# Optimization experiments

Measured on AMD Instinct MI355X. Metric: run time of the kernel, lower is better.

## Reference

```python
import jax, jax.numpy as jnp
import numpy as np

V, H, E = 32000, 8, 32
T, B = 1024, 8

def setup_inputs() -> dict:
    key = jax.random.key(0)
    ks = jax.random.split(key, 11)
    return {
        "x": jax.random.randint(ks[0], (T, B), 0, V),
        "embeddings": jax.random.normal(ks[1], (V, E), jnp.float32),
        "W_x1": jax.random.normal(ks[2], (E, H), jnp.float32),
        "b_x1": jax.random.normal(ks[3], (H,), jnp.float32),
        "W_h1": jax.random.normal(ks[4], (H, H), jnp.float32),
        "b_h1": jax.random.normal(ks[5], (H,), jnp.float32),
        "W_x2": jax.random.normal(ks[6], (E, H), jnp.float32),
        "b_x2": jax.random.normal(ks[7], (H,), jnp.float32),
        "W_h2": jax.random.normal(ks[8], (H, H), jnp.float32),
        "b_h2": jax.random.normal(ks[9], (H,), jnp.float32),
        "output": jax.random.normal(ks[10], (2 * H, V), jnp.float32),
    }

def _run_rnn(xs, Wx, bx, Wh, bh):
    # xs: [T, B, E]. Emit the hidden state BEFORE consuming x_t (matches torch loop:
    # total_h[t] = h, then h = sigmoid(...)). The last update is computed but unused,
    # exactly like the original loop's `break` only skips an unneeded step.
    Bsz = xs.shape[1]
    Hh = Wh.shape[0]
    def step(h, xe):
        h_new = jax.nn.sigmoid(xe @ Wx + bx + h @ Wh + bh)
        return h_new, h
    h0 = jnp.zeros((Bsz, Hh), xs.dtype)
    _, hs = jax.lax.scan(step, h0, xs)
    return hs  # [T, B, H]

def reference(x, embeddings, W_x1, b_x1, W_h1, b_h1, W_x2, b_x2, W_h2, b_h2, output):
    enc = embeddings[x]  # [T, B, E]
    h1 = _run_rnn(enc, W_x1, b_x1, W_h1, b_h1)                       # forward direction
    h2 = jnp.flip(_run_rnn(jnp.flip(enc, 0), W_x2, b_x2, W_h2, b_h2), 0)  # backward direction
    total_h = jnp.concatenate([h1, h2], axis=2)  # [T, B, 2H]
    logits = total_h @ output                    # [T, B, V]
    return jax.nn.log_softmax(logits, axis=2)
```

## Files before the change

### kernel.cpp

```cpp
#include <hip/hip_runtime.h>
#include <math.h>

#if __has_builtin(__builtin_amdgcn_exp2f)
#define EXP2F(x) __builtin_amdgcn_exp2f(x)
#else
#define EXP2F(x) exp2f(x)
#endif

#if __has_builtin(__builtin_amdgcn_logf)
#define LOG2F(x) __builtin_amdgcn_logf(x)
#else
#define LOG2F(x) log2f(x)
#endif

#if __has_builtin(__builtin_amdgcn_rcpf)
#define RCPF(x) __builtin_amdgcn_rcpf(x)
#else
#define RCPF(x) (1.0f / (x))
#endif

#define L2E 1.44269504088896340736f
#define LN2 0.69314718055994530942f

constexpr int V = 32000;
constexpr int H = 8;
constexpr int E = 32;
constexpr int T = 1024;
constexpr int B = 8;
constexpr int TB = T * B;
constexpr int V4 = V / 4;

__global__ __launch_bounds__(256) void proj_kernel(
    const int* __restrict__ x, const float* __restrict__ emb,
    const float* __restrict__ Wx1, const float* __restrict__ bx1,
    const float* __restrict__ bh1,
    const float* __restrict__ Wx2, const float* __restrict__ bx2,
    const float* __restrict__ bh2,
    float* __restrict__ pre1, float* __restrict__ pre2) {
  int i = blockIdx.x * 256 + threadIdx.x;
  int dir = i >> 16;
  int j = i & 65535;
  int h = j & 7;
  int tb = j >> 3;
  int idx = x[tb];
  const float* e = emb + (size_t)idx * E;
  const float* Wx = dir ? Wx2 : Wx1;
  float sum = dir ? (bx2[h] + bh2[h]) : (bx1[h] + bh1[h]);
#pragma unroll
  for (int e0 = 0; e0 < E; ++e0) sum = fmaf(e[e0], Wx[e0 * H + h], sum);
  (dir ? pre2 : pre1)[j] = sum;
}

__global__ __launch_bounds__(128) void rnn_kernel(
    const float* __restrict__ pre1, const float* __restrict__ pre2,
    const float* __restrict__ Wh1, const float* __restrict__ Wh2,
    float* __restrict__ th ) {
  const int tid = threadIdx.x;
  const int dir = tid >> 6;
  const int lane = tid & 63;
  const int b = lane >> 3;
  const int k = lane & 7;
  const float* pre = dir ? pre2 : pre1;
  const float* Wh = dir ? Wh2 : Wh1;

  float w[8];
#pragma unroll
  for (int j = 0; j < 8; ++j) w[j] = Wh[j * H + k];

  float h = 0.f;
  float cur[8], nxt[8];
#pragma unroll
  for (int u = 0; u < 8; ++u) {
    int s = u;
    int tt = dir ? (T - 1 - s) : s;
    cur[u] = pre[tt * 64 + lane];
  }
  for (int blk = 0; blk < T / 8; ++blk) {
    int base = blk * 8;
    if (blk < T / 8 - 1) {
#pragma unroll
      for (int u = 0; u < 8; ++u) {
        int s = base + 8 + u;
        int tt = dir ? (T - 1 - s) : s;
        nxt[u] = pre[tt * 64 + lane];
      }
    }
#pragma unroll
    for (int u = 0; u < 8; ++u) {
      int s = base + u;
      int tt = dir ? (T - 1 - s) : s;
      th[(tt * B + b) * (2 * H) + dir * H + k] = h;
      float acc = cur[u];
#pragma unroll
      for (int j = 0; j < 8; ++j) {
        float hj = __shfl(h, (lane & 56) | j, 64);
        acc = fmaf(hj, w[j], acc);
      }
      h = RCPF(1.0f + EXP2F(acc * -L2E));
    }
#pragma unroll
    for (int u = 0; u < 8; ++u) cur[u] = nxt[u];
  }
}

__global__ __launch_bounds__(256) void logits_kernel(
    const float* __restrict__ th, const float* __restrict__ Wout,
    float* __restrict__ out) {
  const int tid = threadIdx.x;
  const int row0 = blockIdx.x * 16;

  __shared__ float4 th4[16][4];
  __shared__ float red_m[16][4], red_l[16][4];
  __shared__ float sS[16];

  if (tid < 64) {
    th4[tid >> 2][tid & 3] = ((const float4*)th)[row0 * 4 + tid];
  }
  __syncthreads();

  const float4* W4 = (const float4*)Wout;

  float m[16], l[16];
#pragma unroll
  for (int r = 0; r < 16; ++r) { m[r] = -INFINITY; l[r] = 0.f; }

  for (int v4 = tid; v4 < V4; v4 += 256) {
    float4 w[16];
#pragma unroll
    for (int kk = 0; kk < 16; ++kk) w[kk] = W4[(size_t)kk * V4 + v4];
#pragma unroll
    for (int r = 0; r < 16; ++r) {
      float4 c0 = th4[r][0], c1 = th4[r][1], c2 = th4[r][2], c3 = th4[r][3];
      float cc[16] = {c0.x, c0.y, c0.z, c0.w, c1.x, c1.y, c1.z, c1.w,
                      c2.x, c2.y, c2.z, c2.w, c3.x, c3.y, c3.z, c3.w};
      float ax = 0.f, ay = 0.f, az = 0.f, aw = 0.f;
#pragma unroll
      for (int kk = 0; kk < 16; ++kk) {
        ax = fmaf(w[kk].x, cc[kk], ax);
        ay = fmaf(w[kk].y, cc[kk], ay);
        az = fmaf(w[kk].z, cc[kk], az);
        aw = fmaf(w[kk].w, cc[kk], aw);
      }
      float mx = fmaxf(fmaxf(ax, ay), fmaxf(az, aw));
      float nm = fmaxf(m[r], mx);
      float sc = EXP2F((m[r] - nm) * L2E);
      float s = EXP2F((ax - nm) * L2E) + EXP2F((ay - nm) * L2E) +
                EXP2F((az - nm) * L2E) + EXP2F((aw - nm) * L2E);
      l[r] = fmaf(l[r], sc, s);
      m[r] = nm;
    }
  }

  const int wid = tid >> 6, ln = tid & 63;
#pragma unroll
  for (int r = 0; r < 16; ++r) {
    float mm = m[r], ll = l[r];
#pragma unroll
    for (int off = 32; off > 0; off >>= 1) {
      float om = __shfl_xor(mm, off, 64);
      float ol = __shfl_xor(ll, off, 64);
      float nm = fmaxf(mm, om);
      ll = ll * EXP2F((mm - nm) * L2E) + ol * EXP2F((om - nm) * L2E);
      mm = nm;
    }
    if (ln == 0) { red_m[r][wid] = mm; red_l[r][wid] = ll; }
  }
  __syncthreads();
  if (tid < 16) {
    float mm = red_m[tid][0], ll = red_l[tid][0];
#pragma unroll
    for (int i2 = 1; i2 < 4; ++i2) {
      float om = red_m[tid][i2], ol = red_l[tid][i2];
      float nm = fmaxf(mm, om);
      ll = ll * EXP2F((mm - nm) * L2E) + ol * EXP2F((om - nm) * L2E);
      mm = nm;
    }
    sS[tid] = mm + LOG2F(ll) * LN2;
  }
  __syncthreads();

  float4* out4 = (float4*)out;
  for (int v4 = tid; v4 < V4; v4 += 256) {
    float4 w[16];
#pragma unroll
    for (int kk = 0; kk < 16; ++kk) w[kk] = W4[(size_t)kk * V4 + v4];
#pragma unroll
    for (int r = 0; r < 16; ++r) {
      float4 c0 = th4[r][0], c1 = th4[r][1], c2 = th4[r][2], c3 = th4[r][3];
      float cc[16] = {c0.x, c0.y, c0.z, c0.w, c1.x, c1.y, c1.z, c1.w,
                      c2.x, c2.y, c2.z, c2.w, c3.x, c3.y, c3.z, c3.w};
      float ax = 0.f, ay = 0.f, az = 0.f, aw = 0.f;
#pragma unroll
      for (int kk = 0; kk < 16; ++kk) {
        ax = fmaf(w[kk].x, cc[kk], ax);
        ay = fmaf(w[kk].y, cc[kk], ay);
        az = fmaf(w[kk].z, cc[kk], az);
        aw = fmaf(w[kk].w, cc[kk], aw);
      }
      float S = sS[r];
      float4 o;
      o.x = ax - S; o.y = ay - S; o.z = az - S; o.w = aw - S;
      out4[(size_t)(row0 + r) * V4 + v4] = o;
    }
  }
}

extern "C" void kernel_launch(void* const* d_in, const int* in_sizes, int n_in,
                              void* d_out, int out_size, void* d_ws, size_t ws_size,
                              hipStream_t stream) {
  const int* x = (const int*)d_in[0];
  const float* emb = (const float*)d_in[1];
  const float* Wx1 = (const float*)d_in[2];
  const float* bx1 = (const float*)d_in[3];
  const float* Wh1 = (const float*)d_in[4];
  const float* bh1 = (const float*)d_in[5];
  const float* Wx2 = (const float*)d_in[6];
  const float* bx2 = (const float*)d_in[7];
  const float* Wh2 = (const float*)d_in[8];
  const float* bh2 = (const float*)d_in[9];
  const float* Wout = (const float*)d_in[10];
  float* out = (float*)d_out;

  float* ws = (float*)d_ws;
  float* pre1 = ws;
  float* pre2 = ws + TB * H;
  float* th = ws + 2 * TB * H;

  proj_kernel<<<512, 256, 0, stream>>>(x, emb, Wx1, bx1, bh1, Wx2, bx2, bh2,
                                       pre1, pre2);
  rnn_kernel<<<1, 128, 0, stream>>>(pre1, pre2, Wh1, Wh2, th);
  logits_kernel<<<TB / 16, 256, 0, stream>>>(th, Wout, out);
}
```

Baseline: 2.528 ms.

## Compute RNN step per-thread without shuffles, add nontemporal logits stores and occupancy hint

The serial RNN kernel now has each lane hold the whole 8-element hidden state for one batch row. It computes the 8x8 matvec locally instead of exchanging values with 8 cross-lane shuffles per step, and the prefetch depth drops from 8 to 4 steps. The logits kernel gets a min-blocks-per-CU launch bound of 3 and writes its large output with nontemporal stores to avoid polluting cache. The tradeoffs are 8x redundant work across lanes, more register pressure in the RNN kernel, and a possible register spill caused by the launch bound in the logits kernel.

```diff
diff --git a/kernel.cpp b/kernel.cpp
--- a/kernel.cpp
+++ b/kernel.cpp
@@ -21,6 +21,8 @@
 
 #define L2E 1.44269504088896340736f
 #define LN2 0.69314718055994530942f
+
+typedef float floatx4 __attribute__((ext_vector_type(4)));
 
 constexpr int V = 32000;
 constexpr int H = 8;
@@ -58,52 +60,87 @@
   const int tid = threadIdx.x;
   const int dir = tid >> 6;
   const int lane = tid & 63;
-  const int b = lane >> 3;
-  const int k = lane & 7;
-  const float* pre = dir ? pre2 : pre1;
+  const int b = lane & 7;
+  const int sel = (lane >> 3) & 1;
+  const float4* pre4 = (const float4*)(dir ? pre2 : pre1);
   const float* Wh = dir ? Wh2 : Wh1;
-
-  float w[8];
-#pragma unroll
-  for (int j = 0; j < 8; ++j) w[j] = Wh[j * H + k];
-
-  float h = 0.f;
-  float cur[8], nxt[8];
-#pragma unroll
-  for (int u = 0; u < 8; ++u) {
+  float4* th4 = (float4*)th;
+
+  float w[8][8];
+#pragma unroll
+  for (int i = 0; i < 8; ++i)
+#pragma unroll
+    for (int j = 0; j < 8; ++j) w[i][j] = Wh[i * H + j];
+
+  float h0 = 0.f, h1 = 0.f, h2 = 0.f, h3 = 0.f;
+  float h4 = 0.f, h5 = 0.f, h6 = 0.f, h7 = 0.f;
+
+  constexpr int PF = 4;
+  float4 cur[PF][2], nxt[PF][2];
+
+#pragma unroll
+  for (int u = 0; u < PF; ++u) {
     int s = u;
     int tt = dir ? (T - 1 - s) : s;
-    cur[u] = pre[tt * 64 + lane];
-  }
-  for (int blk = 0; blk < T / 8; ++blk) {
-    int base = blk * 8;
-    if (blk < T / 8 - 1) {
-#pragma unroll
-      for (int u = 0; u < 8; ++u) {
-        int s = base + 8 + u;
+    int a = tt * 16 + b * 2;
+    cur[u][0] = pre4[a];
+    cur[u][1] = pre4[a + 1];
+  }
+
+  for (int blk = 0; blk < T / PF; ++blk) {
+    int base = blk * PF;
+    if (blk < T / PF - 1) {
+#pragma unroll
+      for (int u = 0; u < PF; ++u) {
+        int s = base + PF + u;
         int tt = dir ? (T - 1 - s) : s;
-        nxt[u] = pre[tt * 64 + lane];
-      }
-    }
-#pragma unroll
-    for (int u = 0; u < 8; ++u) {
+        int a = tt * 16 + b * 2;
+        nxt[u][0] = pre4[a];
+        nxt[u][1] = pre4[a + 1];
+      }
+    }
+#pragma unroll
+    for (int u = 0; u < PF; ++u) {
       int s = base + u;
       int tt = dir ? (T - 1 - s) : s;
-      th[(tt * B + b) * (2 * H) + dir * H + k] = h;
-      float acc = cur[u];
-#pragma unroll
-      for (int j = 0; j < 8; ++j) {
-        float hj = __shfl(h, (lane & 56) | j, 64);
-        acc = fmaf(hj, w[j], acc);
-      }
-      h = RCPF(1.0f + EXP2F(acc * -L2E));
-    }
-#pragma unroll
-    for (int u = 0; u < 8; ++u) cur[u] = nxt[u];
-  }
-}
-
-__global__ __launch_bounds__(256) void logits_kernel(
+      if (lane < 16) {
+        float4 v = sel ? make_float4(h4, h5, h6, h7)
+                       : make_float4(h0, h1, h2, h3);
+        th4[(tt * B + b) * 4 + dir * 2 + sel] = v;
+      }
+      float a0 = cur[u][0].x, a1 = cur[u][0].y, a2 = cur[u][0].z, a3 = cur[u][0].w;
+      float a4 = cur[u][1].x, a5 = cur[u][1].y, a6 = cur[u][1].z, a7 = cur[u][1].w;
+#pragma unroll
+      for (int i = 0; i < 8; ++i) {
+        float hi = (i == 0) ? h0 : (i == 1) ? h1 : (i == 2) ? h2 : (i == 3) ? h3
+                 : (i == 4) ? h4 : (i == 5) ? h5 : (i == 6) ? h6 : h7;
+        a0 = fmaf(hi, w[i][0], a0);
+        a1 = fmaf(hi, w[i][1], a1);
+        a2 = fmaf(hi, w[i][2], a2);
+        a3 = fmaf(hi, w[i][3], a3);
+        a4 = fmaf(hi, w[i][4], a4);
+        a5 = fmaf(hi, w[i][5], a5);
+        a6 = fmaf(hi, w[i][6], a6);
+        a7 = fmaf(hi, w[i][7], a7);
+      }
+      h0 = RCPF(1.0f + EXP2F(a0 * -L2E));
+      h1 = RCPF(1.0f + EXP2F(a1 * -L2E));
+      h2 = RCPF(1.0f + EXP2F(a2 * -L2E));
+      h3 = RCPF(1.0f + EXP2F(a3 * -L2E));
+      h4 = RCPF(1.0f + EXP2F(a4 * -L2E));
+      h5 = RCPF(1.0f + EXP2F(a5 * -L2E));
+      h6 = RCPF(1.0f + EXP2F(a6 * -L2E));
+      h7 = RCPF(1.0f + EXP2F(a7 * -L2E));
+    }
+#pragma unroll
+    for (int u = 0; u < PF; ++u) {
+      cur[u][0] = nxt[u][0];
+      cur[u][1] = nxt[u][1];
+    }
+  }
+}
+
+__global__ __launch_bounds__(256, 3) void logits_kernel(
     const float* __restrict__ th, const float* __restrict__ Wout,
     float* __restrict__ out) {
   const int tid = threadIdx.x;
@@ -179,7 +216,7 @@
   }
   __syncthreads();
 
-  float4* out4 = (float4*)out;
+  floatx4* out4 = (floatx4*)out;
   for (int v4 = tid; v4 < V4; v4 += 256) {
     float4 w[16];
 #pragma unroll
@@ -198,9 +235,9 @@
         aw = fmaf(w[kk].w, cc[kk], aw);
       }
       float S = sS[r];
-      float4 o;
+      floatx4 o;
       o.x = ax - S; o.y = ay - S; o.z = az - S; o.w = aw - S;
-      out4[(size_t)(row0 + r) * V4 + v4] = o;
+      __builtin_nontemporal_store(o, &out4[(size_t)(row0 + r) * V4 + v4]);
     }
   }
 }
```

New measurement: 4.027 ms. 59.3% more time.
